# Performance work log

Hardware: AMD Instinct MI355X
Metric: run time of the kernel (lower is better)

The kernel has to match this reference:

```python
import jax, jax.numpy as jnp
import numpy as np

T, B, C, H, W = 4, 16, 256, 32, 32
NH = 8  # num_heads
CH = C // NH
N = H * W
EPS = 1e-5

# Heaviside spike with ATan surrogate gradient (spikingjelly default, alpha=2.0)
@jax.custom_vjp
def spike(x):
    return (x >= 0.0).astype(x.dtype)

def _spike_fwd(x):
    return spike(x), x

def _spike_bwd(x, g):
    alpha = 2.0
    return (g * (alpha / 2.0) / (1.0 + (jnp.pi / 2.0 * alpha * x) ** 2),)

spike.defvjp(_spike_fwd, _spike_bwd)

def lif(x_seq, tau, v_th):
    """Multi-step LIF over leading time axis. v_reset=0 hard reset, detach_reset."""
    def step(v, xt):
        h = v + (xt - v) / tau            # charge
        s = spike(h - v_th)               # fire
        v_next = h * (1.0 - jax.lax.stop_gradient(s))  # hard reset to 0, detached
        return v_next, s
    v0 = jnp.zeros_like(x_seq[0])
    _, spikes = jax.lax.scan(step, v0, x_seq)
    return spikes

def bn1d(x, gamma, beta, mean, var):
    # x: [T,B,C,N]; per-channel affine norm (eval-mode BatchNorm1d)
    inv = gamma / jnp.sqrt(var + EPS)
    return (x - mean[None, None, :, None]) * inv[None, None, :, None] + beta[None, None, :, None]

def setup_inputs() -> dict:
    key = jax.random.key(0)
    ks = jax.random.split(key, 16)
    d = {
        'x': jax.random.normal(ks[0], (T, B, C, H, W), jnp.float32),
        'q_w': jax.random.normal(ks[1], (C, C), jnp.float32) * 0.05,
        'q_gamma': jax.random.uniform(ks[2], (C,), jnp.float32),
        'q_beta': jax.random.normal(ks[3], (C,), jnp.float32) * 0.1,
        'q_mean': jax.random.normal(ks[4], (C,), jnp.float32) * 0.1,
        'q_var': jax.random.uniform(ks[5], (C,), jnp.float32) + 0.5,
        'k_w': jax.random.normal(ks[6], (C, C), jnp.float32) * 0.05,
        'k_gamma': jax.random.uniform(ks[7], (C,), jnp.float32),
        'k_beta': jax.random.normal(ks[8], (C,), jnp.float32) * 0.1,
        'k_mean': jax.random.normal(ks[9], (C,), jnp.float32) * 0.1,
        'k_var': jax.random.uniform(ks[10], (C,), jnp.float32) + 0.5,
        'proj_w': jax.random.normal(ks[11], (C, C), jnp.float32) * 0.05,
        'proj_b': jax.random.normal(ks[12], (C,), jnp.float32) * 0.1,
        'p_gamma': jax.random.uniform(ks[13], (C,), jnp.float32),
        'p_beta': jax.random.normal(ks[14], (C,), jnp.float32) * 0.1,
        'p_mean': jax.random.normal(ks[15], (C,), jnp.float32) * 0.1,
        'p_var': jax.random.uniform(jax.random.fold_in(key, 99), (C,), jnp.float32) + 0.5,
    }
    return d

def reference(x, q_w, q_gamma, q_beta, q_mean, q_var,
              k_w, k_gamma, k_beta, k_mean, k_var,
              proj_w, proj_b, p_gamma, p_beta, p_mean, p_var):
    xn = x.reshape(T, B, C, N)  # flatten spatial
    # q branch: 1x1 conv == channel matmul, then BN, then push/pull LIF
    q = bn1d(jnp.einsum('oc,tbcn->tbon', q_w, xn), q_gamma, q_beta, q_mean, q_var)
    qe_s = lif(q, 2.0, 1.0)   # excitatory spikes
    qi_s = lif(-q, 2.0, 1.0)  # inhibitory spikes
    qe = qe_s.reshape(T, B, NH, CH, N)
    qi = qi_s.reshape(T, B, NH, CH, N)
    # k branch
    k = bn1d(jnp.einsum('oc,tbcn->tbon', k_w, xn), k_gamma, k_beta, k_mean, k_var)
    k_s = lif(k, 2.0, 1.0).reshape(T, B, NH, CH, N)
    # push-pull linear attention: sum over head-channel dim, then LIF gate
    qe_sum = jnp.sum(qe, axis=3, keepdims=True)  # [T,B,NH,1,N]
    qi_sum = jnp.sum(qi, axis=3, keepdims=True)
    attn = lif(qe_sum - qi_sum, 2.0, 0.5)        # v_threshold=0.5
    x_one = attn * k_s                            # [T,B,NH,CH,N]
    xo = x_one.reshape(T, B, C, N)
    # projection: 1x1 conv with bias + BN
    p = jnp.einsum('oc,tbcn->tbon', proj_w, xo) + proj_b[None, None, :, None]
    p = bn1d(p, p_gamma, p_beta, p_mean, p_var).reshape(T, B, C, H, W)
    x_final = lif(p, 2.0, 1.0)
    return x_final
```

## Files before the change

### kernel.cpp

```cpp
#include <hip/hip_runtime.h>
#include <math.h>
#include <stdint.h>

#define TT 4
#define BB 16
#define CC 256
#define NN 1024
#define NT 16
#define EPSF 1e-5f
#define EPS_R 6e-5f

typedef __attribute__((ext_vector_type(8))) short short8;
typedef __attribute__((ext_vector_type(4))) float f32x4;
#define MFMA __builtin_amdgcn_mfma_f32_16x16x32_bf16

#define XCH 1040
#define XPL 33280
#define LDS_X 0
#define LDS_XF 99840
#define LDS_TOT 134656

__device__ __forceinline__ uint32_t f2bf(float x) {
  const uint32_t u = __float_as_uint(x);
  return (u + 0x7FFFu + ((u >> 16) & 1u)) >> 16;
}
__device__ __forceinline__ float bf2f(uint32_t b) { return __uint_as_float(b << 16); }

__global__ __launch_bounds__(256)
void wsplit2(const float* __restrict__ qw, const float* __restrict__ kw,
             const float* __restrict__ pw, uint16_t* __restrict__ ws) {
  const int gid = blockIdx.x * 256 + threadIdx.x;
  const int mat = gid >> 13;
  const int ot  = (gid >> 9) & 15;
  const int kk  = (gid >> 6) & 7;
  const int l   = gid & 63;
  const float* w = (mat == 0 ? qw : (mat == 1 ? kw : pw));
  const int o  = ot * 16 + (l & 15);
  const int k0 = kk * 32 + (l >> 4) * 8;
  uint16_t ph[8], pm[8], pl[8];
  #pragma unroll
  for (int j = 0; j < 8; ++j) {
    const float v = w[(size_t)o * CC + k0 + j];
    const uint32_t bh = f2bf(v);
    const float r1 = v - bf2f(bh);
    const uint32_t bm = f2bf(r1);
    const float r2 = r1 - bf2f(bm);
    ph[j] = (uint16_t)bh; pm[j] = (uint16_t)bm; pl[j] = (uint16_t)f2bf(r2);
  }
  const size_t base = ((size_t)mat * 3 * 65536) + ((size_t)ot * 4096) +
                      kk * 512 + l * 8;
  *(uint4*)(ws + base)          = *(const uint4*)ph;
  *(uint4*)(ws + base + 65536)  = *(const uint4*)pm;
  *(uint4*)(ws + base + 131072) = *(const uint4*)pl;
}

__device__ __forceinline__ void lif4m(float q0, float q1, float q2, float q3,
                                      float th, float s[4], float& mg) {
  const float qq[4] = {q0, q1, q2, q3};
  float v = 0.f;
  #pragma unroll
  for (int t = 0; t < 4; ++t) {
    const float h = v + (qq[t] - v) * 0.5f;
    const float d = h - th;
    mg = fminf(mg, fabsf(d));
    const bool f = d >= 0.f;
    s[t] = f ? 1.f : 0.f;
    v = f ? 0.f : h;
  }
}

__device__ __forceinline__ void rescue3(const float* __restrict__ wrow,
                                        const char* lds, int ln, float sv[4]) {
  #pragma unroll
  for (int t = 0; t < 4; ++t) sv[t] = 0.f;
  #pragma unroll 1
  for (int c8 = 0; c8 < 32; ++c8) {
    const float4 wa = *(const float4*)(wrow + c8 * 8);
    const float4 wb = *(const float4*)(wrow + c8 * 8 + 4);
    const float wl_[8] = {wa.x, wa.y, wa.z, wa.w, wb.x, wb.y, wb.z, wb.w};
    #pragma unroll
    for (int t = 0; t < 4; ++t) {
      const int off = c8 * XCH + (t * 16 + ln) * 16;
      const short8 h = *(const short8*)(lds + LDS_X + 0 * XPL + off);
      const short8 m = *(const short8*)(lds + LDS_X + 1 * XPL + off);
      const short8 l = *(const short8*)(lds + LDS_X + 2 * XPL + off);
      float s = sv[t];
      #pragma unroll
      for (int j = 0; j < 8; ++j) {
        const float xv = (bf2f((uint16_t)h[j]) + bf2f((uint16_t)m[j])) +
                         bf2f((uint16_t)l[j]);
        s = fmaf(wl_[j], xv, s);
      }
      sv[t] = s;
    }
  }
}

__device__ __forceinline__ void rescue1(const float* __restrict__ wrow,
                                        const char* lds, int ln, float sv[4]) {
  #pragma unroll
  for (int t = 0; t < 4; ++t) sv[t] = 0.f;
  #pragma unroll 1
  for (int c8 = 0; c8 < 32; ++c8) {
    const float4 wa = *(const float4*)(wrow + c8 * 8);
    const float4 wb = *(const float4*)(wrow + c8 * 8 + 4);
    const float wl_[8] = {wa.x, wa.y, wa.z, wa.w, wb.x, wb.y, wb.z, wb.w};
    #pragma unroll
    for (int t = 0; t < 4; ++t) {
      const int off = c8 * XCH + (t * 16 + ln) * 16;
      const short8 h = *(const short8*)(lds + LDS_X + off);
      float s = sv[t];
      #pragma unroll
      for (int j = 0; j < 8; ++j)
        s = fmaf(wl_[j], bf2f((uint16_t)h[j]), s);
      sv[t] = s;
    }
  }
}

__global__ __launch_bounds__(1024, 4)
void pushpull_mfma6(const float* __restrict__ x,
                    const float* __restrict__ q_w, const float* __restrict__ q_gamma,
                    const float* __restrict__ q_beta, const float* __restrict__ q_mean,
                    const float* __restrict__ q_var,
                    const float* __restrict__ k_w, const float* __restrict__ k_gamma,
                    const float* __restrict__ k_beta, const float* __restrict__ k_mean,
                    const float* __restrict__ k_var,
                    const float* __restrict__ proj_w, const float* __restrict__ proj_b,
                    const float* __restrict__ p_gamma, const float* __restrict__ p_beta,
                    const float* __restrict__ p_mean, const float* __restrict__ p_var,
                    const uint16_t* __restrict__ ws, float* __restrict__ out) {
  __shared__ __align__(16) char lds[LDS_TOT];

  const int tid  = threadIdx.x;
  const int bid  = (int)blockIdx.x;
  const int lid  = ((bid & 7) << 7) | (bid >> 3);
  const int b    = lid >> 6;
  const int n0   = (lid & 63) * NT;
  const int lane = tid & 63;
  const int ln   = tid & 15;
  const int g    = (tid >> 4) & 3;
  const int ot   = tid >> 6;

  float* xf = (float*)(lds + LDS_XF);
  #pragma unroll 1
  for (int hb = 0; hb < 2; ++hb) {
    #pragma unroll
    for (int it = 0; it < 2; ++it) {
      const int idx = it * 1024 + tid;
      const int n4 = (idx & 3) * 4, t = (idx >> 2) & 3, cl = idx >> 4;
      const float4 v = *(const float4*)(
          x + ((size_t)(t * BB + b) * CC + hb * 128 + cl) * NN + n0 + n4);
      *(float4*)(xf + cl * 68 + t * 16 + n4) = v;
    }
    __syncthreads();
    {
      const int chL = tid >> 6, col = tid & 63;
      uint16_t ph[8], pm[8], pl[8];
      #pragma unroll
      for (int j = 0; j < 8; ++j) {
        const float v = xf[(chL * 8 + j) * 68 + col];
        const uint32_t bh = f2bf(v);
        const float r1 = v - bf2f(bh);
        const uint32_t bm = f2bf(r1);
        const float r2 = r1 - bf2f(bm);
        ph[j] = (uint16_t)bh; pm[j] = (uint16_t)bm; pl[j] = (uint16_t)f2bf(r2);
      }
      const int ca = (hb * 16 + chL) * XCH + col * 16;
      *(uint4*)(lds + LDS_X + 0 * XPL + ca) = *(const uint4*)ph;
      *(uint4*)(lds + LDS_X + 1 * XPL + ca) = *(const uint4*)pm;
      *(uint4*)(lds + LDS_X + 2 * XPL + ca) = *(const uint4*)pl;
    }
    __syncthreads();
  }

  const char* wq = (const char*)ws;
  const char* wk = (const char*)ws + 393216;
  const char* wp = (const char*)ws + 786432;

  f32x4 aq[4], ak[4];
  #pragma unroll
  for (int nt = 0; nt < 4; ++nt) { aq[nt] = (f32x4)0.f; ak[nt] = (f32x4)0.f; }

  short8 qA[2], kA[2], qB[2], kB[2];
#define LOADQK(DQ, DK, KK) do {                                               \
    _Pragma("unroll")                                                         \
    for (int p = 0; p < 2; ++p) {                                             \
      const size_t foff = (size_t)p * 131072 + (size_t)ot * 8192 +            \
                          (size_t)(KK) * 1024 + (size_t)lane * 16;            \
      DQ[p] = *(const short8*)(wq + foff);                                    \
      DK[p] = *(const short8*)(wk + foff);                                    \
    }                                                                         \
  } while (0)
#define STEPQK(FQ, FK, KK) do {                                               \
    __builtin_amdgcn_s_setprio(1);                                            \
    _Pragma("unroll")                                                         \
    for (int nt = 0; nt < 4; ++nt) {                                          \
      const int boff = ((KK) * 4 + g) * XCH + (nt * 16 + ln) * 16;            \
      const short8 b0 = *(const short8*)(lds + LDS_X + 0 * XPL + boff);       \
      const short8 b1 = *(const short8*)(lds + LDS_X + 1 * XPL + boff);       \
      aq[nt] = MFMA(FQ[1], b0, aq[nt], 0, 0, 0);                              \
      aq[nt] = MFMA(FQ[0], b1, aq[nt], 0, 0, 0);                              \
      aq[nt] = MFMA(FQ[0], b0, aq[nt], 0, 0, 0);                              \
      ak[nt] = MFMA(FK[1], b0, ak[nt], 0, 0, 0);                              \
      ak[nt] = MFMA(FK[0], b1, ak[nt], 0, 0, 0);                              \
      ak[nt] = MFMA(FK[0], b0, ak[nt], 0, 0, 0);                              \
    }                                                                         \
    __builtin_amdgcn_s_setprio(0);                                            \
  } while (0)

  LOADQK(qA, kA, 0);
  #pragma unroll 1
  for (int kk2 = 0; kk2 < 4; ++kk2) {
    const int kk = kk2 * 2;
    LOADQK(qB, kB, kk + 1);
    STEPQK(qA, kA, kk);
    if (kk2 < 3) LOADQK(qA, kA, kk + 2);
    STEPQK(qB, kB, kk + 1);
  }

  float dsum[4] = {0.f, 0.f, 0.f, 0.f};
  #pragma unroll
  for (int r = 0; r < 4; ++r) {
    const int o = ot * 16 + g * 4 + r;
    const float inv = q_gamma[o] / sqrtf(q_var[o] + EPSF);
    const float mn = q_mean[o], bt = q_beta[o];
    float qv[4];
    #pragma unroll
    for (int t = 0; t < 4; ++t) qv[t] = (aq[t][r] - mn) * inv + bt;
    float se[4], si[4], mg = 1e30f;
    lif4m(qv[0], qv[1], qv[2], qv[3], 1.0f, se, mg);
    lif4m(-qv[0], -qv[1], -qv[2], -qv[3], 1.0f, si, mg);
    if (__builtin_expect(mg < EPS_R, 0)) {
      float qx[4];
      rescue3(q_w + (size_t)o * CC, lds, ln, qx);
      #pragma unroll
      for (int t = 0; t < 4; ++t) qx[t] = (qx[t] - mn) * inv + bt;
      float m2 = 1e30f;
      lif4m(qx[0], qx[1], qx[2], qx[3], 1.0f, se, m2);
      lif4m(-qx[0], -qx[1], -qx[2], -qx[3], 1.0f, si, m2);
    }
    #pragma unroll
    for (int t = 0; t < 4; ++t) dsum[t] += se[t] - si[t];
  }
  #pragma unroll
  for (int t = 0; t < 4; ++t) {
    float v = dsum[t];
    v += __shfl_xor(v, 16);
    v += __shfl_xor(v, 32);
    dsum[t] = v;
  }

  unsigned kb = 0u;
  #pragma unroll
  for (int r = 0; r < 4; ++r) {
    const int o = ot * 16 + g * 4 + r;
    const float inv = k_gamma[o] / sqrtf(k_var[o] + EPSF);
    const float mn = k_mean[o], bt = k_beta[o];
    float kv[4];
    #pragma unroll
    for (int t = 0; t < 4; ++t) kv[t] = (ak[t][r] - mn) * inv + bt;
    float sk[4], mg = 1e30f;
    lif4m(kv[0], kv[1], kv[2], kv[3], 1.0f, sk, mg);
    if (__builtin_expect(mg < EPS_R, 0)) {
      float kx[4];
      rescue3(k_w + (size_t)o * CC, lds, ln, kx);
      #pragma unroll
      for (int t = 0; t < 4; ++t) kx[t] = (kx[t] - mn) * inv + bt;
      float m2 = 1e30f;
      lif4m(kx[0], kx[1], kx[2], kx[3], 1.0f, sk, m2);
    }
    #pragma unroll
    for (int t = 0; t < 4; ++t) kb |= (sk[t] != 0.f) ? (1u << (r * 4 + t)) : 0u;
  }

  float* db = (float*)(lds + LDS_XF);
  __syncthreads();
  if (g == 0) {
    #pragma unroll
    for (int t = 0; t < 4; ++t) db[(ot * 16 + ln) * 4 + t] = dsum[t];
  }
  __syncthreads();
  float at[4];
  {
    float tot[4];
    #pragma unroll
    for (int t = 0; t < 4; ++t)
      tot[t] = dsum[t] + db[((ot ^ 1) * 16 + ln) * 4 + t];
    float mgd = 1e30f;
    lif4m(tot[0], tot[1], tot[2], tot[3], 0.5f, at, mgd);
  }

  {
    const int chunk = ot * 2 + (g >> 1);
    const int j0 = (g & 1) * 4;
    #pragma unroll
    for (int t = 0; t < 4; ++t) {
      unsigned long long wbits = 0ull;
      #pragma unroll
      for (int r = 0; r < 4; ++r)
        if (((kb >> (r * 4 + t)) & 1u) && at[t] != 0.f)
          wbits |= 0x3F80ull << (r * 16);
      *(unsigned long long*)(lds + LDS_X + chunk * XCH +
                             (t * 16 + ln) * 16 + j0 * 2) = wbits;
    }
  }
  __syncthreads();

  f32x4 ap[4];
  #pragma unroll
  for (int nt = 0; nt < 4; ++nt) ap[nt] = (f32x4)0.f;

  short8 pA[2], pB[2];
#define LOADP(DP, KK) do {                                                    \
    _Pragma("unroll")                                                         \
    for (int p = 0; p < 2; ++p)                                               \
      DP[p] = *(const short8*)(wp + (size_t)p * 131072 + (size_t)ot * 8192 +  \
                               (size_t)(KK) * 1024 + (size_t)lane * 16);      \
  } while (0)
#define STEPP(FP, KK) do {                                                    \
    __builtin_amdgcn_s_setprio(1);                                            \
    _Pragma("unroll")                                                         \
    for (int nt = 0; nt < 4; ++nt) {                                          \
      const short8 b0 = *(const short8*)(lds + LDS_X +                        \
                        ((KK) * 4 + g) * XCH + (nt * 16 + ln) * 16);          \
      ap[nt] = MFMA(FP[1], b0, ap[nt], 0, 0, 0);                              \
      ap[nt] = MFMA(FP[0], b0, ap[nt], 0, 0, 0);                              \
    }                                                                         \
    __builtin_amdgcn_s_setprio(0);                                            \
  } while (0)

  LOADP(pA, 0);
  #pragma unroll 1
  for (int kk2 = 0; kk2 < 4; ++kk2) {
    const int kk = kk2 * 2;
    LOADP(pB, kk + 1);
    STEPP(pA, kk);
    if (kk2 < 3) LOADP(pA, kk + 2);
    STEPP(pB, kk + 1);
  }

  #pragma unroll
  for (int r = 0; r < 4; ++r) {
    const int o = ot * 16 + g * 4 + r;
    const float inv = p_gamma[o] / sqrtf(p_var[o] + EPSF);
    const float mn = p_mean[o], bt = p_beta[o], pb = proj_b[o];
    float pv[4];
    #pragma unroll
    for (int t = 0; t < 4; ++t) pv[t] = ((ap[t][r] + pb) - mn) * inv + bt;
    float sp[4], mg = 1e30f;
    lif4m(pv[0], pv[1], pv[2], pv[3], 1.0f, sp, mg);
    if (__builtin_expect(mg < EPS_R, 0)) {
      float px[4];
      rescue1(proj_w + (size_t)o * CC, lds, ln, px);
      #pragma unroll
      for (int t = 0; t < 4; ++t) px[t] = ((px[t] + pb) - mn) * inv + bt;
      float m2 = 1e30f;
      lif4m(px[0], px[1], px[2], px[3], 1.0f, sp, m2);
    }
    #pragma unroll
    for (int t = 0; t < 4; ++t)
      out[((size_t)(t * BB + b) * CC + o) * NN + n0 + ln] = sp[t];
  }
}

extern "C" void kernel_launch(void* const* d_in, const int* in_sizes, int n_in,
                              void* d_out, int out_size, void* d_ws, size_t ws_size,
                              hipStream_t stream) {
  const float* x       = (const float*)d_in[0];
  const float* q_w     = (const float*)d_in[1];
  const float* q_gamma = (const float*)d_in[2];
  const float* q_beta  = (const float*)d_in[3];
  const float* q_mean  = (const float*)d_in[4];
  const float* q_var   = (const float*)d_in[5];
  const float* k_w     = (const float*)d_in[6];
  const float* k_gamma = (const float*)d_in[7];
  const float* k_beta  = (const float*)d_in[8];
  const float* k_mean  = (const float*)d_in[9];
  const float* k_var   = (const float*)d_in[10];
  const float* proj_w  = (const float*)d_in[11];
  const float* proj_b  = (const float*)d_in[12];
  const float* p_gamma = (const float*)d_in[13];
  const float* p_beta  = (const float*)d_in[14];
  const float* p_mean  = (const float*)d_in[15];
  const float* p_var   = (const float*)d_in[16];
  float* out = (float*)d_out;
  uint16_t* wsp = (uint16_t*)d_ws;

  wsplit2<<<96, 256, 0, stream>>>(q_w, k_w, proj_w, wsp);
  pushpull_mfma6<<<BB * (NN / NT), 1024, 0, stream>>>(
      x, q_w, q_gamma, q_beta, q_mean, q_var,
      k_w, k_gamma, k_beta, k_mean, k_var,
      proj_w, proj_b, p_gamma, p_beta, p_mean, p_var, wsp, out);
}
```

Baseline: 126.0 us.

## Drop third bf16 split plane from LDS and rescue from global fp32 input

Removes the low bf16 residual plane of x from shared memory and keeps only high and mid planes, which the MFMA path already uses. The rare near-threshold rescue path now recomputes the dot product directly from global fp32 x instead of the three LDS planes. Staging changes to 8 passes of 32 channels with a smaller fp32 buffer. Together these shrink LDS from about 134KB to about 75KB, which could allow two 1024-thread blocks per CU. The cost is more staging barriers and a slow, uncoalesced global rescue loop when it triggers.

```diff
diff --git a/kernel.cpp b/kernel.cpp
--- a/kernel.cpp
+++ b/kernel.cpp
@@ -17,8 +17,8 @@
 #define XCH 1040
 #define XPL 33280
 #define LDS_X 0
-#define LDS_XF 99840
-#define LDS_TOT 134656
+#define LDS_XF 66560
+#define LDS_TOT 75008
 
 __device__ __forceinline__ uint32_t f2bf(float x) {
   const uint32_t u = __float_as_uint(x);
@@ -69,7 +69,20 @@
   }
 }
 
-__device__ __forceinline__ void rescue3(const float* __restrict__ wrow,
+__device__ __forceinline__ void rescue3g(const float* __restrict__ wrow,
+                                         const float* __restrict__ x,
+                                         int b, int n0, int ln, float sv[4]) {
+  #pragma unroll
+  for (int t = 0; t < 4; ++t) {
+    const float* xg = x + (size_t)(t * BB + b) * CC * NN + n0 + ln;
+    float s = 0.f;
+    #pragma unroll 1
+    for (int c = 0; c < CC; ++c) s = fmaf(wrow[c], xg[(size_t)c * NN], s);
+    sv[t] = s;
+  }
+}
+
+__device__ __forceinline__ void rescue1(const float* __restrict__ wrow,
                                         const char* lds, int ln, float sv[4]) {
   #pragma unroll
   for (int t = 0; t < 4; ++t) sv[t] = 0.f;
@@ -81,33 +94,6 @@
     #pragma unroll
     for (int t = 0; t < 4; ++t) {
       const int off = c8 * XCH + (t * 16 + ln) * 16;
-      const short8 h = *(const short8*)(lds + LDS_X + 0 * XPL + off);
-      const short8 m = *(const short8*)(lds + LDS_X + 1 * XPL + off);
-      const short8 l = *(const short8*)(lds + LDS_X + 2 * XPL + off);
-      float s = sv[t];
-      #pragma unroll
-      for (int j = 0; j < 8; ++j) {
-        const float xv = (bf2f((uint16_t)h[j]) + bf2f((uint16_t)m[j])) +
-                         bf2f((uint16_t)l[j]);
-        s = fmaf(wl_[j], xv, s);
-      }
-      sv[t] = s;
-    }
-  }
-}
-
-__device__ __forceinline__ void rescue1(const float* __restrict__ wrow,
-                                        const char* lds, int ln, float sv[4]) {
-  #pragma unroll
-  for (int t = 0; t < 4; ++t) sv[t] = 0.f;
-  #pragma unroll 1
-  for (int c8 = 0; c8 < 32; ++c8) {
-    const float4 wa = *(const float4*)(wrow + c8 * 8);
-    const float4 wb = *(const float4*)(wrow + c8 * 8 + 4);
-    const float wl_[8] = {wa.x, wa.y, wa.z, wa.w, wb.x, wb.y, wb.z, wb.w};
-    #pragma unroll
-    for (int t = 0; t < 4; ++t) {
-      const int off = c8 * XCH + (t * 16 + ln) * 16;
       const short8 h = *(const short8*)(lds + LDS_X + off);
       float s = sv[t];
       #pragma unroll
@@ -119,7 +105,7 @@
 }
 
 __global__ __launch_bounds__(1024, 4)
-void pushpull_mfma6(const float* __restrict__ x,
+void pushpull_mfma9(const float* __restrict__ x,
                     const float* __restrict__ q_w, const float* __restrict__ q_gamma,
                     const float* __restrict__ q_beta, const float* __restrict__ q_mean,
                     const float* __restrict__ q_var,
@@ -144,32 +130,27 @@
 
   float* xf = (float*)(lds + LDS_XF);
   #pragma unroll 1
-  for (int hb = 0; hb < 2; ++hb) {
-    #pragma unroll
-    for (int it = 0; it < 2; ++it) {
-      const int idx = it * 1024 + tid;
-      const int n4 = (idx & 3) * 4, t = (idx >> 2) & 3, cl = idx >> 4;
+  for (int ps = 0; ps < 8; ++ps) {
+    if (tid < 512) {
+      const int cl = tid >> 4, t = (tid >> 2) & 3, n4 = (tid & 3) * 4;
       const float4 v = *(const float4*)(
-          x + ((size_t)(t * BB + b) * CC + hb * 128 + cl) * NN + n0 + n4);
-      *(float4*)(xf + cl * 68 + t * 16 + n4) = v;
+          x + ((size_t)(t * BB + b) * CC + ps * 32 + cl) * NN + n0 + n4);
+      *(float4*)(xf + cl * 66 + t * 16 + n4) = v;
     }
     __syncthreads();
-    {
+    if (tid < 256) {
       const int chL = tid >> 6, col = tid & 63;
-      uint16_t ph[8], pm[8], pl[8];
+      uint16_t ph[8], pm[8];
       #pragma unroll
       for (int j = 0; j < 8; ++j) {
-        const float v = xf[(chL * 8 + j) * 68 + col];
+        const float v = xf[(chL * 8 + j) * 66 + col];
         const uint32_t bh = f2bf(v);
-        const float r1 = v - bf2f(bh);
-        const uint32_t bm = f2bf(r1);
-        const float r2 = r1 - bf2f(bm);
-        ph[j] = (uint16_t)bh; pm[j] = (uint16_t)bm; pl[j] = (uint16_t)f2bf(r2);
+        pm[j] = (uint16_t)f2bf(v - bf2f(bh));
+        ph[j] = (uint16_t)bh;
       }
-      const int ca = (hb * 16 + chL) * XCH + col * 16;
-      *(uint4*)(lds + LDS_X + 0 * XPL + ca) = *(const uint4*)ph;
-      *(uint4*)(lds + LDS_X + 1 * XPL + ca) = *(const uint4*)pm;
-      *(uint4*)(lds + LDS_X + 2 * XPL + ca) = *(const uint4*)pl;
+      const int ca = (ps * 4 + chL) * XCH + col * 16;
+      *(uint4*)(lds + LDS_X + ca) = *(const uint4*)ph;
+      *(uint4*)(lds + LDS_X + XPL + ca) = *(const uint4*)pm;
     }
     __syncthreads();
   }
@@ -197,8 +178,8 @@
     _Pragma("unroll")                                                         \
     for (int nt = 0; nt < 4; ++nt) {                                          \
       const int boff = ((KK) * 4 + g) * XCH + (nt * 16 + ln) * 16;            \
-      const short8 b0 = *(const short8*)(lds + LDS_X + 0 * XPL + boff);       \
-      const short8 b1 = *(const short8*)(lds + LDS_X + 1 * XPL + boff);       \
+      const short8 b0 = *(const short8*)(lds + LDS_X + boff);                 \
+      const short8 b1 = *(const short8*)(lds + LDS_X + XPL + boff);           \
       aq[nt] = MFMA(FQ[1], b0, aq[nt], 0, 0, 0);                              \
       aq[nt] = MFMA(FQ[0], b1, aq[nt], 0, 0, 0);                              \
       aq[nt] = MFMA(FQ[0], b0, aq[nt], 0, 0, 0);                              \
@@ -233,7 +214,7 @@
     lif4m(-qv[0], -qv[1], -qv[2], -qv[3], 1.0f, si, mg);
     if (__builtin_expect(mg < EPS_R, 0)) {
       float qx[4];
-      rescue3(q_w + (size_t)o * CC, lds, ln, qx);
+      rescue3g(q_w + (size_t)o * CC, x, b, n0, ln, qx);
       #pragma unroll
       for (int t = 0; t < 4; ++t) qx[t] = (qx[t] - mn) * inv + bt;
       float m2 = 1e30f;
@@ -264,7 +245,7 @@
     lif4m(kv[0], kv[1], kv[2], kv[3], 1.0f, sk, mg);
     if (__builtin_expect(mg < EPS_R, 0)) {
       float kx[4];
-      rescue3(k_w + (size_t)o * CC, lds, ln, kx);
+      rescue3g(k_w + (size_t)o * CC, x, b, n0, ln, kx);
       #pragma unroll
       for (int t = 0; t < 4; ++t) kx[t] = (kx[t] - mn) * inv + bt;
       float m2 = 1e30f;
@@ -388,7 +369,7 @@
   uint16_t* wsp = (uint16_t*)d_ws;
 
   wsplit2<<<96, 256, 0, stream>>>(q_w, k_w, proj_w, wsp);
-  pushpull_mfma6<<<BB * (NN / NT), 1024, 0, stream>>>(
+  pushpull_mfma9<<<BB * (NN / NT), 1024, 0, stream>>>(
       x, q_w, q_gamma, q_beta, q_mean, q_var,
       k_w, k_gamma, k_beta, k_mean, k_var,
       proj_w, proj_b, p_gamma, p_beta, p_mean, p_var, wsp, out);
```

Result: slower. 449.0 us (+256.4%).
